# Kernel tuning notes

Measured on AMD Instinct MI355X. Metric: run time of the kernel, lower is better.

Reference implementation:

```python
import math
import jax, jax.numpy as jnp
import numpy as np

PRED_LEN = 96
K = 32
LOW_FREQ = 1


def setup_inputs() -> dict:
    key = jax.random.key(0)
    x = jax.random.normal(key, (8, 512, 512), dtype=jnp.float32)
    return {"x": x}


def _fourier_forward(x):
    b, t, d = x.shape
    # rFFT over time axis (always fp32, matching torch autocast-disabled block)
    x_freq = jnp.fft.rfft(x.astype(jnp.float32), axis=1)  # (b, t//2+1, d) complex64
    freqs = jnp.fft.rfftfreq(t).astype(jnp.float32)
    if t % 2 == 0:
        x_freq = x_freq[:, LOW_FREQ:-1]
        f = freqs[LOW_FREQ:-1]
    else:
        x_freq = x_freq[:, LOW_FREQ:]
        f = freqs[LOW_FREQ:]
    n_freq = x_freq.shape[1]
    k = min(K, n_freq)

    # top-k |X(f)| independently per (batch, channel): move freq to last axis
    mag = jnp.transpose(jnp.abs(x_freq), (0, 2, 1))          # (b, d, f)
    _, idx = jax.lax.top_k(mag, k)                            # (b, d, k)
    x_freq_t = jnp.transpose(x_freq, (0, 2, 1))               # (b, d, f)
    x_sel = jnp.transpose(jnp.take_along_axis(x_freq_t, idx, axis=2), (0, 2, 1))  # (b, k, d)
    f_sel = jnp.transpose(f[idx], (0, 2, 1))[:, :, None, :]   # (b, k, 1, d)

    # extrapolate: add conjugate (negative) frequencies
    x_full = jnp.concatenate([x_sel, jnp.conj(x_sel)], axis=1)  # (b, 2k, d)
    f_full = jnp.concatenate([f_sel, -f_sel], axis=1)           # (b, 2k, 1, d)
    t_val = jnp.arange(t + PRED_LEN, dtype=jnp.float32)[None, None, :, None]  # (1,1,T,1)
    amp = (jnp.abs(x_full) / t)[:, :, None, :]                  # (b, 2k, 1, d)
    phase = jnp.angle(x_full)[:, :, None, :]                    # (b, 2k, 1, d)
    x_time = amp * jnp.cos(2.0 * math.pi * f_full * t_val + phase)  # (b, 2k, T, d)
    return jnp.sum(x_time, axis=1)                              # (b, t+pred_len, d)


def reference(x):
    return _fourier_forward(x)
```

## Files before the change

kernel.cpp:

```cpp
#include <hip/hip_runtime.h>
#include <math.h>

#define BATCH 8
#define TLEN  512
#define DDIM  512
#define TOUT  608
#define KSEL  32
#define DT    8

#define TWO_PI_OVER_512 0.0122718463030851562f
#define SC (2.0f / 512.0f)

typedef __attribute__((ext_vector_type(8))) short short8;
typedef __attribute__((ext_vector_type(4))) float f32x4;

#define BMT_OFF 0
#define WK_OFF  4194304

__device__ __forceinline__ unsigned short f2bf(float f) {
    unsigned u = __float_as_uint(f);
    return (unsigned short)((u + 0x7FFF + ((u >> 16) & 1)) >> 16);
}

__device__ __constant__ const float CC16[16] = {
     1.f,  0.92387953251128674f,  0.70710678118654752f,  0.38268343236508977f,
     0.f, -0.38268343236508977f, -0.70710678118654752f, -0.92387953251128674f,
    -1.f, -0.92387953251128674f, -0.70710678118654752f, -0.38268343236508977f,
     0.f,  0.38268343236508977f,  0.70710678118654752f,  0.92387953251128674f };
__device__ __constant__ const float SS16[16] = {
     0.f,  0.38268343236508977f,  0.70710678118654752f,  0.92387953251128674f,
     1.f,  0.92387953251128674f,  0.70710678118654752f,  0.38268343236508977f,
     0.f, -0.38268343236508977f, -0.70710678118654752f, -0.92387953251128674f,
    -1.f, -0.92387953251128674f, -0.70710678118654752f, -0.38268343236508977f };

__global__ __launch_bounds__(512, 4) void fft_topk_kernel(const float* __restrict__ x,
                                                          unsigned short* __restrict__ BmT,
                                                          unsigned short* __restrict__ Wk) {
    __shared__ __align__(16) unsigned char smem[42328];
    float2* Xl  = (float2*)smem;
    float*  xs  = (float*)smem;
    float*  ysr = (float*)(smem + 16448);
    float*  ysi = (float*)(smem + 27140);
    float2* tw  = (float2*)(smem + 37832);

    const int tid = threadIdx.x;
    const int bid = blockIdx.x;
    const int b   = bid >> 6;
    const int d0  = ((bid & 7) * 8 + ((bid >> 3) & 7)) * DT;

    {
        float s, c;
        sincosf((float)tid * TWO_PI_OVER_512, &s, &c);
        tw[tid] = make_float2(c, s);
    }

    {
        const float* xr = x + ((size_t)b * TLEN + tid) * DDIM + d0;
        float4 lo = *(const float4*)(xr);
        float4 hi = *(const float4*)(xr + 4);
        *(float4*)&xs[tid * 8]     = lo;
        *(float4*)&xs[tid * 8 + 4] = hi;
    }
    __syncthreads();

    {
        const int h   = tid >> 8;
        const int rem = tid & 255;
        const int aA  = rem >> 3;
        const int dA  = rem & 7;
        float xv[16];
        #pragma unroll
        for (int c = 0; c < 16; ++c)
            xv[c] = xs[(aA + 32 * c) * 8 + dA];

        if (h == 0) {
            #pragma unroll
            for (int q = 0; q <= 4; ++q) {
                float sr = 0.f, si = 0.f;
                #pragma unroll
                for (int c = 0; c < 16; ++c) {
                    const int n = (c * q) & 15;
                    sr = fmaf(xv[c],  CC16[n], sr);
                    si = fmaf(xv[c], -SS16[n], si);
                }
                ysr[(q * 33 + aA) * 9 + dA] = sr;
                ysi[(q * 33 + aA) * 9 + dA] = si;
            }
        } else {
            #pragma unroll
            for (int q = 5; q <= 8; ++q) {
                float sr = 0.f, si = 0.f;
                #pragma unroll
                for (int c = 0; c < 16; ++c) {
                    const int n = (c * q) & 15;
                    sr = fmaf(xv[c],  CC16[n], sr);
                    si = fmaf(xv[c], -SS16[n], si);
                }
                ysr[(q * 33 + aA) * 9 + dA] = sr;
                ysi[(q * 33 + aA) * 9 + dA] = si;
            }
        }
    }
    __syncthreads();

    {
        const int ahalf = tid & 1;
        const int dB    = (tid >> 1) & 7;
        const int kk    = tid >> 4;
        const int qp    = kk & 15;
        const int qrow  = (qp <= 8) ? qp : 16 - qp;
        const bool neg  = (qp > 8);

        const int ybase = (qrow * 33 + ahalf * 16) * 9 + dB;
        float Yr_[16], Yi_[16], Pr_[16], Pi_[16];
        #pragma unroll
        for (int aa = 0; aa < 16; ++aa) {
            Yr_[aa] = ysr[ybase + aa * 9];
            float yi = ysi[ybase + aa * 9];
            Yi_[aa] = neg ? -yi : yi;
        }
        #pragma unroll
        for (int aa = 0; aa < 16; ++aa) {
            const int arow = ahalf * 16 + aa;
            float2 w = tw[(arow * kk) & 511];
            Pr_[aa] = w.x;
            Pi_[aa] = -w.y;
        }

        float ar[8] = {}, ai[8] = {};
        #pragma unroll
        for (int aa = 0; aa < 16; ++aa) {
            float zr = Yr_[aa] * Pr_[aa] - Yi_[aa] * Pi_[aa];
            float zi = Yr_[aa] * Pi_[aa] + Yi_[aa] * Pr_[aa];
            #pragma unroll
            for (int u = 0; u < 8; ++u) {
                const int n = (aa * u) & 15;
                ar[u] = fmaf(zr, CC16[n], fmaf(zi,  SS16[n], ar[u]));
                ai[u] = fmaf(zi, CC16[n], fmaf(-zr, SS16[n], ai[u]));
            }
        }

        #pragma unroll
        for (int u = 0; u < 8; ++u) {
            ar[u] += __shfl_xor(ar[u], 1);
            ai[u] += __shfl_xor(ai[u], 1);
        }
        #pragma unroll
        for (int v = 0; v < 4; ++v) {
            const int u = ahalf * 4 + v;
            Xl[dB * 257 + kk + 32 * u] = make_float2(ar[u], ai[u]);
        }
    }
    __syncthreads();

    if (tid < 256) {
        float2 w = tw[(bid * tid) & 511];
        unsigned val = (unsigned)f2bf(w.x * SC) | ((unsigned)f2bf(-w.y * SC) << 16);
        *(unsigned*)&Wk[((size_t)bid << 9) + 2 * tid] = val;
    }

    {
        const int l  = tid & 63;
        const int dd = tid >> 6;
        const unsigned long long below = ((unsigned long long)1 << l) - 1;

        float zr[4], zi[4];
        unsigned vb[4];
        int mm[4];
        #pragma unroll
        for (int s = 0; s < 4; ++s) {
            int m = 1 + l + 64 * s;
            mm[s] = m;
            if (m <= 255) {
                float2 z = Xl[dd * 257 + m];
                zr[s] = z.x; zi[s] = z.y;
                vb[s] = __float_as_uint(fmaf(z.x, z.x, z.y * z.y));
            } else { zr[s] = 0.f; zi[s] = 0.f; vb[s] = 0u; }
        }

        unsigned tau = 0;
        #pragma unroll
        for (int bit = 29; bit >= 1; bit -= 2) {
            const unsigned c1 = tau | (1u << bit);
            const unsigned c2 = tau | (2u << bit);
            const unsigned c3 = tau | (3u << bit);
            int n1 = __popcll(__ballot(vb[0] >= c1)) + __popcll(__ballot(vb[1] >= c1))
                   + __popcll(__ballot(vb[2] >= c1)) + __popcll(__ballot(vb[3] >= c1));
            int n2 = __popcll(__ballot(vb[0] >= c2)) + __popcll(__ballot(vb[1] >= c2))
                   + __popcll(__ballot(vb[2] >= c2)) + __popcll(__ballot(vb[3] >= c2));
            int n3 = __popcll(__ballot(vb[0] >= c3)) + __popcll(__ballot(vb[1] >= c3))
                   + __popcll(__ballot(vb[2] >= c3)) + __popcll(__ballot(vb[3] >= c3));
            tau = (n3 >= KSEL) ? c3 : (n2 >= KSEL) ? c2 : (n1 >= KSEL) ? c1 : tau;
        }
        {
            const unsigned c = tau | 1u;
            int n = __popcll(__ballot(vb[0] >= c)) + __popcll(__ballot(vb[1] >= c))
                  + __popcll(__ballot(vb[2] >= c)) + __popcll(__ballot(vb[3] >= c));
            if (n >= KSEL) tau = c;
        }

        unsigned long long beq[4];
        int cgt = 0;
        #pragma unroll
        for (int s = 0; s < 4; ++s) {
            beq[s] = __ballot(vb[s] == tau);
            cgt += __popcll(__ballot(vb[s] > tau));
        }
        const int need = KSEL - cgt;

        unsigned short* Brow = BmT + ((size_t)(b * DDIM + d0 + dd) << 9);
        int be = 0;
        #pragma unroll
        for (int s = 0; s < 4; ++s) {
            bool keep = (vb[s] > tau);
            if (vb[s] == tau) {
                int r = be + __popcll(beq[s] & below);
                keep = (r < need);
            }
            be += __popcll(beq[s]);
            unsigned val = keep ? ((unsigned)f2bf(zr[s]) | ((unsigned)f2bf(zi[s]) << 16)) : 0u;
            int mi = mm[s] & 255;
            *(unsigned*)(Brow + 2 * mi) = val;
        }
    }
}

__global__ __launch_bounds__(512, 4) void gemm_kernel(const unsigned short* __restrict__ Wk,
                                                      const unsigned short* __restrict__ BmT,
                                                      float* __restrict__ out) {
    __shared__ unsigned short Al[64][136];
    __shared__ unsigned short Bl[64][136];

    const int tid = threadIdx.x;
    const int bid = blockIdx.x;
    const int bt  = bid >> 6;
    const int b   = (bid >> 3) & 7;
    const int bd  = bid & 7;

    const int wid  = tid >> 6;
    const int l    = tid & 63;
    const int wm   = wid & 3;
    const int wn   = wid >> 2;
    const int lrow = l & 15;
    const int lk8  = (l >> 4) * 8;

    const int srow = tid >> 3;
    const int soff = (tid & 7) * 8;

    const unsigned short* Wrow = Wk  + (size_t)(bt * 64 + srow) * 512 + soff;
    const unsigned short* Brow = BmT + ((size_t)(b * DDIM + bd * 64 + srow)) * 512 + soff;

    f32x4 acc0 = {0.f, 0.f, 0.f, 0.f};
    f32x4 acc1 = {0.f, 0.f, 0.f, 0.f};

    uint4 av0 = *(const uint4*)(Wrow);
    uint4 av1 = *(const uint4*)(Wrow + 64);
    uint4 bv0 = *(const uint4*)(Brow);
    uint4 bv1 = *(const uint4*)(Brow + 64);

    for (int kc = 0; kc < 512; kc += 128) {
        __syncthreads();
        *(uint4*)&Al[srow][soff]      = av0;
        *(uint4*)&Al[srow][soff + 64] = av1;
        *(uint4*)&Bl[srow][soff]      = bv0;
        *(uint4*)&Bl[srow][soff + 64] = bv1;
        __syncthreads();

        if (kc + 128 < 512) {
            av0 = *(const uint4*)(Wrow + kc + 128);
            av1 = *(const uint4*)(Wrow + kc + 192);
            bv0 = *(const uint4*)(Brow + kc + 128);
            bv1 = *(const uint4*)(Brow + kc + 192);
        }

        #pragma unroll
        for (int ks = 0; ks < 4; ++ks) {
            short8 af  = *(const short8*)&Al[wm * 16 + lrow][ks * 32 + lk8];
            short8 bf0 = *(const short8*)&Bl[wn * 32 + lrow][ks * 32 + lk8];
            short8 bf1 = *(const short8*)&Bl[wn * 32 + 16 + lrow][ks * 32 + lk8];
            acc0 = __builtin_amdgcn_mfma_f32_16x16x32_bf16(af, bf0, acc0, 0, 0, 0);
            acc1 = __builtin_amdgcn_mfma_f32_16x16x32_bf16(af, bf1, acc1, 0, 0, 0);
        }
    }

    const int tg = bt * 64 + wm * 16 + (l >> 4) * 4;
    const int dg = bd * 64 + wn * 32 + (l & 15);
    float* ob = out + (size_t)b * TOUT * DDIM;
    #pragma unroll
    for (int r = 0; r < 4; ++r) {
        const int t = tg + r;
        ob[(size_t)t * DDIM + dg]      = acc0[r];
        ob[(size_t)t * DDIM + dg + 16] = acc1[r];
        if (t < 96) {
            ob[(size_t)(t + 512) * DDIM + dg]      = acc0[r];
            ob[(size_t)(t + 512) * DDIM + dg + 16] = acc1[r];
        }
    }
}

extern "C" void kernel_launch(void* const* d_in, const int* in_sizes, int n_in,
                              void* d_out, int out_size, void* d_ws, size_t ws_size,
                              hipStream_t stream) {
    const float* x   = (const float*)d_in[0];
    float*       out = (float*)d_out;
    unsigned short* BmT = (unsigned short*)((char*)d_ws + BMT_OFF);
    unsigned short* Wk  = (unsigned short*)((char*)d_ws + WK_OFF);

    fft_topk_kernel<<<BATCH * 64, 512, 0, stream>>>(x, BmT, Wk);
    gemm_kernel<<<BATCH * 64, 512, 0, stream>>>(Wk, BmT, out);
}
```

Measured before the change: 23.65 us.

## Exploit time-reversal symmetry to halve GEMM rows via cos/sin split

Splits the twiddle and spectrum layout into separate cosine and sine halves so one GEMM pass over t in [0,256) yields both t and 512-t outputs, using a sign-flipped copy of the A fragment for the sine half. The GEMM grid drops to 256 blocks, and the t=256 row is computed separately as a warp-reduced alternating-sign dot product inside the FFT kernel. This halves the twiddle matrix size and GEMM block count at the cost of doubling the MFMA work per block and adding scattered 16-bit stores.

```diff
diff --git a/kernel.cpp b/kernel.cpp
--- a/kernel.cpp
+++ b/kernel.cpp
@@ -35,7 +35,8 @@
 
 __global__ __launch_bounds__(512, 4) void fft_topk_kernel(const float* __restrict__ x,
                                                           unsigned short* __restrict__ BmT,
-                                                          unsigned short* __restrict__ Wk) {
+                                                          unsigned short* __restrict__ Wk,
+                                                          float* __restrict__ out) {
     __shared__ __align__(16) unsigned char smem[42328];
     float2* Xl  = (float2*)smem;
     float*  xs  = (float*)smem;
@@ -153,10 +154,15 @@
     }
     __syncthreads();
 
-    if (tid < 256) {
-        float2 w = tw[(bid * tid) & 511];
-        unsigned val = (unsigned)f2bf(w.x * SC) | ((unsigned)f2bf(-w.y * SC) << 16);
-        *(unsigned*)&Wk[((size_t)bid << 9) + 2 * tid] = val;
+    if (bid < 256 && tid < 256) {
+        const int half = tid >> 7;
+        const int j    = tid & 127;
+        float2 w0 = tw[(bid * (2 * j)) & 511];
+        float2 w1 = tw[(bid * (2 * j + 1)) & 511];
+        unsigned val = half
+            ? ((unsigned)f2bf(w0.y * SC) | ((unsigned)f2bf(w1.y * SC) << 16))
+            : ((unsigned)f2bf(w0.x * SC) | ((unsigned)f2bf(w1.x * SC) << 16));
+        *(unsigned*)&Wk[((size_t)bid << 9) + (half << 8) + 2 * j] = val;
     }
 
     {
@@ -210,6 +216,7 @@
 
         unsigned short* Brow = BmT + ((size_t)(b * DDIM + d0 + dd) << 9);
         int be = 0;
+        float dot = 0.f;
         #pragma unroll
         for (int s = 0; s < 4; ++s) {
             bool keep = (vb[s] > tau);
@@ -218,10 +225,17 @@
                 keep = (r < need);
             }
             be += __popcll(beq[s]);
-            unsigned val = keep ? ((unsigned)f2bf(zr[s]) | ((unsigned)f2bf(zi[s]) << 16)) : 0u;
-            int mi = mm[s] & 255;
-            *(unsigned*)(Brow + 2 * mi) = val;
-        }
+            const int mi = mm[s] & 255;
+            Brow[mi]       = keep ? f2bf(zr[s]) : (unsigned short)0;
+            Brow[256 + mi] = keep ? f2bf(zi[s]) : (unsigned short)0;
+            if (keep) dot = fmaf(zr[s], (mm[s] & 1) ? -SC : SC, dot);
+        }
+
+        #pragma unroll
+        for (int off = 1; off < 64; off <<= 1)
+            dot += __shfl_xor(dot, off);
+        if (l == 0)
+            out[((size_t)b * TOUT + 256) * DDIM + d0 + dd] = dot;
     }
 }
 
@@ -250,8 +264,10 @@
     const unsigned short* Wrow = Wk  + (size_t)(bt * 64 + srow) * 512 + soff;
     const unsigned short* Brow = BmT + ((size_t)(b * DDIM + bd * 64 + srow)) * 512 + soff;
 
-    f32x4 acc0 = {0.f, 0.f, 0.f, 0.f};
-    f32x4 acc1 = {0.f, 0.f, 0.f, 0.f};
+    f32x4 accp0 = {0.f, 0.f, 0.f, 0.f};
+    f32x4 accp1 = {0.f, 0.f, 0.f, 0.f};
+    f32x4 accm0 = {0.f, 0.f, 0.f, 0.f};
+    f32x4 accm1 = {0.f, 0.f, 0.f, 0.f};
 
     uint4 av0 = *(const uint4*)(Wrow);
     uint4 av1 = *(const uint4*)(Wrow + 64);
@@ -278,8 +294,13 @@
             short8 af  = *(const short8*)&Al[wm * 16 + lrow][ks * 32 + lk8];
             short8 bf0 = *(const short8*)&Bl[wn * 32 + lrow][ks * 32 + lk8];
             short8 bf1 = *(const short8*)&Bl[wn * 32 + 16 + lrow][ks * 32 + lk8];
-            acc0 = __builtin_amdgcn_mfma_f32_16x16x32_bf16(af, bf0, acc0, 0, 0, 0);
-            acc1 = __builtin_amdgcn_mfma_f32_16x16x32_bf16(af, bf1, acc1, 0, 0, 0);
+            const bool is_sin = (kc + ks * 32) >= 256;
+            short8 afm = af;
+            if (is_sin) afm ^= (short8)(short)0x8000;
+            accp0 = __builtin_amdgcn_mfma_f32_16x16x32_bf16(af,  bf0, accp0, 0, 0, 0);
+            accp1 = __builtin_amdgcn_mfma_f32_16x16x32_bf16(af,  bf1, accp1, 0, 0, 0);
+            accm0 = __builtin_amdgcn_mfma_f32_16x16x32_bf16(afm, bf0, accm0, 0, 0, 0);
+            accm1 = __builtin_amdgcn_mfma_f32_16x16x32_bf16(afm, bf1, accm1, 0, 0, 0);
         }
     }
 
@@ -288,12 +309,15 @@
     float* ob = out + (size_t)b * TOUT * DDIM;
     #pragma unroll
     for (int r = 0; r < 4; ++r) {
-        const int t = tg + r;
-        ob[(size_t)t * DDIM + dg]      = acc0[r];
-        ob[(size_t)t * DDIM + dg + 16] = acc1[r];
+        const int t  = tg + r;
+        const int rp = 512 - t;
+        ob[(size_t)t * DDIM + dg]       = accm0[r];
+        ob[(size_t)t * DDIM + dg + 16]  = accm1[r];
+        ob[(size_t)rp * DDIM + dg]      = accp0[r];
+        ob[(size_t)rp * DDIM + dg + 16] = accp1[r];
         if (t < 96) {
-            ob[(size_t)(t + 512) * DDIM + dg]      = acc0[r];
-            ob[(size_t)(t + 512) * DDIM + dg + 16] = acc1[r];
+            ob[(size_t)(t + 512) * DDIM + dg]      = accm0[r];
+            ob[(size_t)(t + 512) * DDIM + dg + 16] = accm1[r];
         }
     }
 }
@@ -306,6 +330,6 @@
     unsigned short* BmT = (unsigned short*)((char*)d_ws + BMT_OFF);
     unsigned short* Wk  = (unsigned short*)((char*)d_ws + WK_OFF);
 
-    fft_topk_kernel<<<BATCH * 64, 512, 0, stream>>>(x, BmT, Wk);
-    gemm_kernel<<<BATCH * 64, 512, 0, stream>>>(Wk, BmT, out);
+    fft_topk_kernel<<<BATCH * 64, 512, 0, stream>>>(x, BmT, Wk, out);
+    gemm_kernel<<<256, 512, 0, stream>>>(Wk, BmT, out);
 }
```

Measured after the change: 22.97 us. 1.03x faster.
